# Performance work log

Hardware: AMD Instinct MI355X
Metric: run time of the kernel (lower is better)

## Reference

```python
import jax, jax.numpy as jnp
import numpy as np

# CombinedBoundaryLoss constants
W_DICE, W_FOCAL, W_HD = 1.0, 0.5, 0.1
F_ALPHA, F_GAMMA, F_BW = 0.25, 2.0, 3.0      # FocalBoundaryLoss
D_SMOOTH, D_BW = 1e-5, 2.0                    # SoftDiceBoundaryLoss
HD_TEMP = 0.01                                # SoftHausdorffLoss


def detect_edges(mask):
    # 3x3 Laplacian, padding=1 (SAME), NCHW
    k = jnp.array([[0., 1., 0.], [1., -4., 1.], [0., 1., 0.]], mask.dtype)[None, None]
    return jax.lax.conv_general_dilated(
        mask, k, window_strides=(1, 1), padding='SAME',
        dimension_numbers=('NCHW', 'OIHW', 'NCHW'))


def setup_inputs() -> dict:
    key = jax.random.key(0)
    k1, k2 = jax.random.split(key)
    B, H, W = 4, 96, 96
    pred = jax.random.normal(k1, (B, 1, H, W), dtype=jnp.float32)
    target = jax.random.randint(k2, (B, 1, H, W), 0, 2).astype(jnp.float32)
    return {"pred": pred, "target": target}


def reference(pred, target):
    B, _, H, W = pred.shape
    dt = pred.dtype
    prob = jax.nn.sigmoid(pred)
    edge = detect_edges(target)
    edge_mask = (jnp.abs(edge) > 0).astype(dt)  # (B,1,H,W)

    # ---- SoftDiceBoundaryLoss ----
    inter = (prob * target).sum(axis=(1, 2, 3))
    p_sum = prob.sum(axis=(1, 2, 3))
    t_sum = target.sum(axis=(1, 2, 3))
    dice_all = (2 * inter + D_SMOOTH) / (p_sum + t_sum + D_SMOOTH)
    loss_all = 1.0 - dice_all.mean()
    inter_e = (prob * edge_mask).sum(axis=(1, 2, 3))
    te_sum = edge_mask.sum(axis=(1, 2, 3))
    dice_e = (2 * inter_e + D_SMOOTH) / (inter_e + te_sum + D_SMOOTH)
    loss_edge = jnp.where(edge_mask.sum() > 0, 1.0 - dice_e.mean(), 0.0)
    dice_loss = loss_all + D_BW * loss_edge

    # ---- FocalBoundaryLoss ----
    # stable BCE-with-logits, elementwise
    ce = jnp.maximum(pred, 0) - pred * target + jnp.log1p(jnp.exp(-jnp.abs(pred)))
    p_t = prob * target + (1 - prob) * (1 - target)
    focal = F_ALPHA * (1 - p_t) ** F_GAMMA * ce
    focal_loss = ((1.0 + F_BW * edge_mask) * focal).mean()

    # ---- SoftHausdorffLoss (receives RAW LOGITS, as in the source) ----
    y = jnp.arange(H, dtype=dt)
    x = jnp.arange(W, dtype=dt)
    gy, gx = jnp.meshgrid(y, x, indexing='ij')
    coords = jnp.stack([gx.ravel(), gy.ravel()], axis=1)          # (N,2)
    sq = (coords ** 2).sum(axis=1)                                 # (N,)
    dists_sq = jnp.maximum(sq[:, None] + sq[None, :] - 2.0 * (coords @ coords.T), 0.0)  # (N,N)
    neg_inf = jnp.array(-jnp.inf, dt)

    def per_item(args):
        p_flat, t_flat = args                                      # (N,), (N,)
        m = t_flat > 0.5
        mf = m.astype(dt)
        # softmin over target columns only (masked softmax)
        logits = -dists_sq / HD_TEMP + jnp.where(m, 0.0, neg_inf)[None, :]
        wts = jax.nn.softmax(logits, axis=1)                       # (N,N)
        # coords/dists are constants w.r.t. pred in the source (torch.no_grad)
        min_dists_p = jax.lax.stop_gradient((wts * dists_sq).sum(axis=1))  # (N,)
        loss_p = (p_flat * min_dists_p).sum()
        # target->pred term: min over ALL grid points (always 0, kept for faithfulness)
        col_min = dists_sq.min(axis=0)                             # (N,)
        loss_t = (col_min * mf).sum() / jnp.maximum(mf.sum(), 1.0)
        return jnp.where(m.any(), loss_p + loss_t, 0.0)

    hd_per_b = jax.lax.map(per_item, (pred.reshape(B, -1), target.reshape(B, -1)))
    hd_loss = hd_per_b.sum() / B

    return W_DICE * dice_loss + W_FOCAL * focal_loss + W_HD * hd_loss
```

## Files before the change

### kernel.cpp

```cpp
#include <hip/hip_runtime.h>

#define BATCH 4
#define IMH 96
#define IMW 96
#define NPIX (IMH * IMW)
#define CHUNKS (NPIX / 256)
#define NBLK (BATCH * CHUNKS)

__device__ __forceinline__ float block_reduce_sum(float v, float* smem) {
    int lane = threadIdx.x & 63;
    int wid  = threadIdx.x >> 6;
    #pragma unroll
    for (int o = 32; o > 0; o >>= 1) v += __shfl_down(v, o, 64);
    if (lane == 0) smem[wid] = v;
    __syncthreads();
    float r = 0.f;
    if (threadIdx.x == 0) {
        #pragma unroll
        for (int w = 0; w < 4; ++w) r += smem[w];
    }
    __syncthreads();
    return r;
}

__global__ void fused_kernel(const float* __restrict__ pred,
                             const float* __restrict__ target,
                             float* __restrict__ ws) {
    __shared__ float smem[4];
    int blk   = blockIdx.x;
    int b     = blk / CHUNKS;
    int chunk = blk - b * CHUNKS;
    const float* p = pred + b * NPIX;
    const float* t = target + b * NPIX;

    int i  = chunk * 256 + (int)threadIdx.x;
    int py = i / IMW, px = i - py * IMW;
    float tv = t[i], pv = p[i];
    float prob = 1.f / (1.f + expf(-pv));

    float lap = -4.f * tv;
    lap += (py > 0)       ? t[i - IMW] : 0.f;
    lap += (py < IMH - 1) ? t[i + IMW] : 0.f;
    lap += (px > 0)       ? t[i - 1]   : 0.f;
    lap += (px < IMW - 1) ? t[i + 1]   : 0.f;
    float em = (lap != 0.f) ? 1.f : 0.f;

    float ce = fmaxf(pv, 0.f) - pv * tv + log1pf(expf(-fabsf(pv)));
    float pt = prob * tv + (1.f - prob) * (1.f - tv);
    float om = 1.f - pt;
    float fsum = (1.f + 3.f * em) * (0.25f * om * om * ce);

    int best = (tv > 0.5f) ? 0 : 0x7fffffff;
    for (int r = 1; r <= 95; ++r) {
        int rr = r * r;
        if (__all(best <= rr)) break;
        if (best > rr) {
            int y0 = py - r, y1 = py + r, x0 = px - r, x1 = px + r;
            for (int xx = x0; xx <= x1; ++xx) {
                if ((unsigned)xx < (unsigned)IMW) {
                    int dx = xx - px, dd = dx * dx + rr;
                    if ((unsigned)y0 < (unsigned)IMH && t[y0 * IMW + xx] > 0.5f) best = min(best, dd);
                    if ((unsigned)y1 < (unsigned)IMH && t[y1 * IMW + xx] > 0.5f) best = min(best, dd);
                }
            }
            for (int yy = y0 + 1; yy <= y1 - 1; ++yy) {
                if ((unsigned)yy < (unsigned)IMH) {
                    int dy = yy - py, dd = dy * dy + rr;
                    if ((unsigned)x0 < (unsigned)IMW && t[yy * IMW + x0] > 0.5f) best = min(best, dd);
                    if ((unsigned)x1 < (unsigned)IMW && t[yy * IMW + x1] > 0.5f) best = min(best, dd);
                }
            }
        }
    }
    float hd_val = (best == 0x7fffffff) ? 0.f : pv * (float)best;

    float* wsb = ws + blk * 8;
    float r;
    r = block_reduce_sum(prob * tv, smem); if (threadIdx.x == 0) wsb[0] = r;
    r = block_reduce_sum(prob,      smem); if (threadIdx.x == 0) wsb[1] = r;
    r = block_reduce_sum(tv,        smem); if (threadIdx.x == 0) wsb[2] = r;
    r = block_reduce_sum(prob * em, smem); if (threadIdx.x == 0) wsb[3] = r;
    r = block_reduce_sum(em,        smem); if (threadIdx.x == 0) wsb[4] = r;
    r = block_reduce_sum(fsum,      smem); if (threadIdx.x == 0) wsb[5] = r;
    r = block_reduce_sum(hd_val,    smem); if (threadIdx.x == 0) wsb[6] = r;
}

__global__ void finalize_kernel(const float* __restrict__ ws, float* __restrict__ out) {
    __shared__ float simg[BATCH][8];
    int tid  = threadIdx.x;
    int wid  = tid >> 6;
    int lane = tid & 63;
    float v0 = 0.f, v1 = 0.f, v2 = 0.f, v3 = 0.f, v4 = 0.f, v5 = 0.f, v6 = 0.f;
    if (lane < CHUNKS) {
        const float* w = ws + (wid * CHUNKS + lane) * 8;
        v0 = w[0]; v1 = w[1]; v2 = w[2]; v3 = w[3]; v4 = w[4]; v5 = w[5]; v6 = w[6];
    }
    #pragma unroll
    for (int o = 32; o > 0; o >>= 1) {
        v0 += __shfl_down(v0, o, 64); v1 += __shfl_down(v1, o, 64);
        v2 += __shfl_down(v2, o, 64); v3 += __shfl_down(v3, o, 64);
        v4 += __shfl_down(v4, o, 64); v5 += __shfl_down(v5, o, 64);
        v6 += __shfl_down(v6, o, 64);
    }
    if (lane == 0) {
        simg[wid][0] = v0; simg[wid][1] = v1; simg[wid][2] = v2; simg[wid][3] = v3;
        simg[wid][4] = v4; simg[wid][5] = v5; simg[wid][6] = v6;
    }
    __syncthreads();
    if (tid == 0) {
        float dice_all_sum = 0.f, dice_e_sum = 0.f, te_total = 0.f, fsum = 0.f, hd = 0.f;
        for (int b = 0; b < BATCH; ++b) {
            float inter   = simg[b][0];
            float psum    = simg[b][1];
            float tsum    = simg[b][2];
            float inter_e = simg[b][3];
            float tesum   = simg[b][4];
            fsum += simg[b][5];
            hd   += simg[b][6];
            dice_all_sum += (2.f * inter + 1e-5f) / (psum + tsum + 1e-5f);
            dice_e_sum   += (2.f * inter_e + 1e-5f) / (inter_e + tesum + 1e-5f);
            te_total += tesum;
        }
        float loss_all  = 1.f - dice_all_sum * 0.25f;
        float loss_edge = (te_total > 0.f) ? (1.f - dice_e_sum * 0.25f) : 0.f;
        float dice_loss = loss_all + 2.0f * loss_edge;
        float focal_loss = fsum / (float)(BATCH * NPIX);
        float hd_loss = hd * 0.25f;
        out[0] = 1.0f * dice_loss + 0.5f * focal_loss + 0.1f * hd_loss;
    }
}

extern "C" void kernel_launch(void* const* d_in, const int* in_sizes, int n_in,
                              void* d_out, int out_size, void* d_ws, size_t ws_size,
                              hipStream_t stream) {
    const float* pred   = (const float*)d_in[0];
    const float* target = (const float*)d_in[1];
    float* out = (float*)d_out;
    float* ws  = (float*)d_ws;

    hipLaunchKernelGGL(fused_kernel,    dim3(NBLK), dim3(256), 0, stream, pred, target, ws);
    hipLaunchKernelGGL(finalize_kernel, dim3(1),    dim3(256), 0, stream, ws, out);
}
```

Baseline: 15.07 us.

## Preload 5x5 target window for Laplacian and nearest-target search; batch block reductions

Each thread loads a 5x5 neighbourhood of the target into registers. That window serves both the Laplacian edge mask and the first two rings of the nearest-target distance search, and the ring loop only runs if some lane in the wavefront has no target within distance 3. The seven separate block reductions, each with two barriers, become one interleaved shuffle reduction with a single barrier. The window adds 25 loads and extra register pressure per thread.

```diff
diff --git a/kernel.cpp b/kernel.cpp
--- a/kernel.cpp
+++ b/kernel.cpp
@@ -7,26 +7,10 @@
 #define CHUNKS (NPIX / 256)
 #define NBLK (BATCH * CHUNKS)
 
-__device__ __forceinline__ float block_reduce_sum(float v, float* smem) {
-    int lane = threadIdx.x & 63;
-    int wid  = threadIdx.x >> 6;
-    #pragma unroll
-    for (int o = 32; o > 0; o >>= 1) v += __shfl_down(v, o, 64);
-    if (lane == 0) smem[wid] = v;
-    __syncthreads();
-    float r = 0.f;
-    if (threadIdx.x == 0) {
-        #pragma unroll
-        for (int w = 0; w < 4; ++w) r += smem[w];
-    }
-    __syncthreads();
-    return r;
-}
-
-__global__ void fused_kernel(const float* __restrict__ pred,
-                             const float* __restrict__ target,
-                             float* __restrict__ ws) {
-    __shared__ float smem[4];
+__global__ void __launch_bounds__(256) fused_kernel(const float* __restrict__ pred,
+                                                    const float* __restrict__ target,
+                                                    float* __restrict__ ws) {
+    __shared__ float smem[4][8];
     int blk   = blockIdx.x;
     int b     = blk / CHUNKS;
     int chunk = blk - b * CHUNKS;
@@ -35,76 +19,104 @@
 
     int i  = chunk * 256 + (int)threadIdx.x;
     int py = i / IMW, px = i - py * IMW;
-    float tv = t[i], pv = p[i];
+    float pv = p[i];
+
+    float w[5][5];
+    #pragma unroll
+    for (int dy = -2; dy <= 2; ++dy) {
+        int yy = py + dy;
+        bool yok = (unsigned)yy < (unsigned)IMH;
+        #pragma unroll
+        for (int dx = -2; dx <= 2; ++dx) {
+            int xx = px + dx;
+            bool ok = yok && ((unsigned)xx < (unsigned)IMW);
+            w[dy + 2][dx + 2] = ok ? t[yy * IMW + xx] : 0.f;
+        }
+    }
+    float tv = w[2][2];
+
+    float lap = w[1][2] + w[3][2] + w[2][1] + w[2][3] - 4.f * tv;
+    float em  = (lap != 0.f) ? 1.f : 0.f;
+
     float prob = 1.f / (1.f + expf(-pv));
-
-    float lap = -4.f * tv;
-    lap += (py > 0)       ? t[i - IMW] : 0.f;
-    lap += (py < IMH - 1) ? t[i + IMW] : 0.f;
-    lap += (px > 0)       ? t[i - 1]   : 0.f;
-    lap += (px < IMW - 1) ? t[i + 1]   : 0.f;
-    float em = (lap != 0.f) ? 1.f : 0.f;
-
     float ce = fmaxf(pv, 0.f) - pv * tv + log1pf(expf(-fabsf(pv)));
     float pt = prob * tv + (1.f - prob) * (1.f - tv);
     float om = 1.f - pt;
     float fsum = (1.f + 3.f * em) * (0.25f * om * om * ce);
 
-    int best = (tv > 0.5f) ? 0 : 0x7fffffff;
-    for (int r = 1; r <= 95; ++r) {
-        int rr = r * r;
-        if (__all(best <= rr)) break;
-        if (best > rr) {
-            int y0 = py - r, y1 = py + r, x0 = px - r, x1 = px + r;
-            for (int xx = x0; xx <= x1; ++xx) {
-                if ((unsigned)xx < (unsigned)IMW) {
-                    int dx = xx - px, dd = dx * dx + rr;
-                    if ((unsigned)y0 < (unsigned)IMH && t[y0 * IMW + xx] > 0.5f) best = min(best, dd);
-                    if ((unsigned)y1 < (unsigned)IMH && t[y1 * IMW + xx] > 0.5f) best = min(best, dd);
+    int best = 0x7fffffff;
+    #pragma unroll
+    for (int dy = -2; dy <= 2; ++dy)
+        #pragma unroll
+        for (int dx = -2; dx <= 2; ++dx)
+            if (w[dy + 2][dx + 2] > 0.5f) best = min(best, dy * dy + dx * dx);
+
+    if (!__all(best <= 9)) {
+        for (int r = 3; r <= 95; ++r) {
+            int rr = r * r;
+            if (__all(best <= rr)) break;
+            if (best > rr) {
+                int y0 = py - r, y1 = py + r, x0 = px - r, x1 = px + r;
+                for (int xx = x0; xx <= x1; ++xx) {
+                    if ((unsigned)xx < (unsigned)IMW) {
+                        int dx = xx - px, dd = dx * dx + rr;
+                        if ((unsigned)y0 < (unsigned)IMH && t[y0 * IMW + xx] > 0.5f) best = min(best, dd);
+                        if ((unsigned)y1 < (unsigned)IMH && t[y1 * IMW + xx] > 0.5f) best = min(best, dd);
+                    }
                 }
-            }
-            for (int yy = y0 + 1; yy <= y1 - 1; ++yy) {
-                if ((unsigned)yy < (unsigned)IMH) {
-                    int dy = yy - py, dd = dy * dy + rr;
-                    if ((unsigned)x0 < (unsigned)IMW && t[yy * IMW + x0] > 0.5f) best = min(best, dd);
-                    if ((unsigned)x1 < (unsigned)IMW && t[yy * IMW + x1] > 0.5f) best = min(best, dd);
+                for (int yy = y0 + 1; yy <= y1 - 1; ++yy) {
+                    if ((unsigned)yy < (unsigned)IMH) {
+                        int dy = yy - py, dd = dy * dy + rr;
+                        if ((unsigned)x0 < (unsigned)IMW && t[yy * IMW + x0] > 0.5f) best = min(best, dd);
+                        if ((unsigned)x1 < (unsigned)IMW && t[yy * IMW + x1] > 0.5f) best = min(best, dd);
+                    }
                 }
             }
         }
     }
     float hd_val = (best == 0x7fffffff) ? 0.f : pv * (float)best;
 
-    float* wsb = ws + blk * 8;
-    float r;
-    r = block_reduce_sum(prob * tv, smem); if (threadIdx.x == 0) wsb[0] = r;
-    r = block_reduce_sum(prob,      smem); if (threadIdx.x == 0) wsb[1] = r;
-    r = block_reduce_sum(tv,        smem); if (threadIdx.x == 0) wsb[2] = r;
-    r = block_reduce_sum(prob * em, smem); if (threadIdx.x == 0) wsb[3] = r;
-    r = block_reduce_sum(em,        smem); if (threadIdx.x == 0) wsb[4] = r;
-    r = block_reduce_sum(fsum,      smem); if (threadIdx.x == 0) wsb[5] = r;
-    r = block_reduce_sum(hd_val,    smem); if (threadIdx.x == 0) wsb[6] = r;
+    float vals[7] = { prob * tv, prob, tv, prob * em, em, fsum, hd_val };
+    int lane = threadIdx.x & 63;
+    int wid  = threadIdx.x >> 6;
+    #pragma unroll
+    for (int o = 32; o > 0; o >>= 1) {
+        #pragma unroll
+        for (int k = 0; k < 7; ++k) vals[k] += __shfl_down(vals[k], o, 64);
+    }
+    if (lane == 0) {
+        #pragma unroll
+        for (int k = 0; k < 7; ++k) smem[wid][k] = vals[k];
+    }
+    __syncthreads();
+    if (threadIdx.x == 0) {
+        float* wsb = ws + blk * 8;
+        #pragma unroll
+        for (int k = 0; k < 7; ++k)
+            wsb[k] = smem[0][k] + smem[1][k] + smem[2][k] + smem[3][k];
+    }
 }
 
-__global__ void finalize_kernel(const float* __restrict__ ws, float* __restrict__ out) {
+__global__ void __launch_bounds__(256) finalize_kernel(const float* __restrict__ ws,
+                                                       float* __restrict__ out) {
     __shared__ float simg[BATCH][8];
     int tid  = threadIdx.x;
     int wid  = tid >> 6;
     int lane = tid & 63;
-    float v0 = 0.f, v1 = 0.f, v2 = 0.f, v3 = 0.f, v4 = 0.f, v5 = 0.f, v6 = 0.f;
+    float v[7] = {0.f, 0.f, 0.f, 0.f, 0.f, 0.f, 0.f};
     if (lane < CHUNKS) {
         const float* w = ws + (wid * CHUNKS + lane) * 8;
-        v0 = w[0]; v1 = w[1]; v2 = w[2]; v3 = w[3]; v4 = w[4]; v5 = w[5]; v6 = w[6];
+        #pragma unroll
+        for (int k = 0; k < 7; ++k) v[k] = w[k];
     }
     #pragma unroll
     for (int o = 32; o > 0; o >>= 1) {
-        v0 += __shfl_down(v0, o, 64); v1 += __shfl_down(v1, o, 64);
-        v2 += __shfl_down(v2, o, 64); v3 += __shfl_down(v3, o, 64);
-        v4 += __shfl_down(v4, o, 64); v5 += __shfl_down(v5, o, 64);
-        v6 += __shfl_down(v6, o, 64);
+        #pragma unroll
+        for (int k = 0; k < 7; ++k) v[k] += __shfl_down(v[k], o, 64);
     }
     if (lane == 0) {
-        simg[wid][0] = v0; simg[wid][1] = v1; simg[wid][2] = v2; simg[wid][3] = v3;
-        simg[wid][4] = v4; simg[wid][5] = v5; simg[wid][6] = v6;
+        #pragma unroll
+        for (int k = 0; k < 7; ++k) simg[wid][k] = v[k];
     }
     __syncthreads();
     if (tid == 0) {
```

Measured after the change: 12.81 us (median of 2 runs). 15.0% less time.
